# Kernel optimization log

Measured on AMD Instinct MI355X. Metric: run time of the kernel, lower is better.

The kernel has to match this reference:

```python
import jax, jax.numpy as jnp
import numpy as np

NUM_TOKENS = 16384
HIDDEN = 4096
NUM_EXPERTS = 64
TOP_K = 8


def setup_inputs() -> dict:
    key = jax.random.key(0)
    k1, k2 = jax.random.split(key)
    x = jax.random.normal(k1, (NUM_TOKENS, HIDDEN), dtype=jnp.float32)
    # nn.Linear default init scale ~ 1/sqrt(fan_in); keep logits well-scaled
    gate_w = jax.random.normal(k2, (NUM_EXPERTS, HIDDEN), dtype=jnp.float32) / jnp.sqrt(jnp.float32(HIDDEN))
    gate_b = jnp.zeros((NUM_EXPERTS,), dtype=jnp.float32)
    return {"x": x, "gate_w": gate_w, "gate_b": gate_b}


def reference(x, gate_w, gate_b):
    # gate linear: (T, H) @ (H, E) + (E,) -> (T, E)
    g = jnp.einsum("th,eh->te", x, gate_w) + gate_b
    # top-k over experts (sorted descending, like torch.topk)
    top_vals, top_idx = jax.lax.top_k(g, TOP_K)  # (T, K) each
    # softmax over the k selected logits
    expert_weights = jax.nn.softmax(top_vals, axis=-1)
    return expert_weights, top_idx
```

## Files before the change

### kernel.cpp

```cpp
#include <hip/hip_runtime.h>
#include <math.h>


#define NUM_TOKENS 16384
#define HID 4096
#define NE 64
#define TOPK 8
#define BT 32
#define BK 64
#define WSTRIDE 66

__global__ __launch_bounds__(256, 2)
void gating_kernel(const float* __restrict__ x,
                   const float* __restrict__ gw,
                   const float* __restrict__ gb,
                   float* __restrict__ out) {
    __shared__ double ws_d[NE][WSTRIDE];
    __shared__ double xs_d[BT][WSTRIDE];

    const int tid  = threadIdx.x;
    const int tok0 = blockIdx.x * BT;

    const int e0 = tid & 15;
    const int t2 = (tid >> 4) * 2;

    double acc[2][4];
#pragma unroll
    for (int i = 0; i < 2; i++)
#pragma unroll
        for (int j = 0; j < 4; j++) acc[i][j] = 0.0;

    for (int k0 = 0; k0 < HID; k0 += BK) {
#pragma unroll
        for (int i = 0; i < 2; i++) {
            int idx = i * 256 + tid;
            int tt  = idx >> 4;
            int cc  = (idx & 15) << 2;
            float4 v = *(const float4*)(x + (size_t)(tok0 + tt) * HID + k0 + cc);
            xs_d[tt][cc + 0] = (double)v.x;
            xs_d[tt][cc + 1] = (double)v.y;
            xs_d[tt][cc + 2] = (double)v.z;
            xs_d[tt][cc + 3] = (double)v.w;
        }
#pragma unroll
        for (int i = 0; i < 4; i++) {
            int idx = i * 256 + tid;
            int ee  = idx >> 4;
            int cc  = (idx & 15) << 2;
            float4 v = *(const float4*)(gw + (size_t)ee * HID + k0 + cc);
            ws_d[ee][cc + 0] = (double)v.x;
            ws_d[ee][cc + 1] = (double)v.y;
            ws_d[ee][cc + 2] = (double)v.z;
            ws_d[ee][cc + 3] = (double)v.w;
        }
        __syncthreads();

        const double* xr0 = &xs_d[t2 + 0][0];
        const double* xr1 = &xs_d[t2 + 1][0];
        const double* w0  = &ws_d[e0 +  0][0];
        const double* w1  = &ws_d[e0 + 16][0];
        const double* w2  = &ws_d[e0 + 32][0];
        const double* w3  = &ws_d[e0 + 48][0];

#pragma unroll 8
        for (int kk = 0; kk < BK; kk++) {
            double xa = xr0[kk], xb = xr1[kk];
            double a0 = w0[kk], a1 = w1[kk], a2 = w2[kk], a3 = w3[kk];
            acc[0][0] = fma(xa, a0, acc[0][0]);
            acc[0][1] = fma(xa, a1, acc[0][1]);
            acc[0][2] = fma(xa, a2, acc[0][2]);
            acc[0][3] = fma(xa, a3, acc[0][3]);
            acc[1][0] = fma(xb, a0, acc[1][0]);
            acc[1][1] = fma(xb, a1, acc[1][1]);
            acc[1][2] = fma(xb, a2, acc[1][2]);
            acc[1][3] = fma(xb, a3, acc[1][3]);
        }
        __syncthreads();
    }

    double* lg = &ws_d[0][0];
#pragma unroll
    for (int i = 0; i < 2; i++) {
        int t = t2 + i;
#pragma unroll
        for (int j = 0; j < 4; j++) {
            int e = e0 + 16 * j;
            lg[t * 65 + e] = acc[i][j] + (double)gb[e];
        }
    }
    __syncthreads();

    const int wv = tid >> 6, ln = tid & 63;
    if (ln < 8) {
        int t = wv * 8 + ln;
        const double* row = lg + t * 65;
        unsigned long long sel = 0ull;
        double vals[TOPK];
        int idxs[TOPK];
#pragma unroll
        for (int k = 0; k < TOPK; k++) {
            double bv = -1e300;
            int bi = 0;
            for (int e = 0; e < NE; e++) {
                bool valid = !((sel >> e) & 1ull);
                double v = row[e];
                bool take = valid && (v > bv);
                bv = take ? v : bv;
                bi = take ? e : bi;
            }
            sel |= 1ull << bi;
            vals[k] = bv;
            idxs[k] = bi;
        }
        double m = vals[0];
        float ex[TOPK];
        float s = 0.f;
#pragma unroll
        for (int k = 0; k < TOPK; k++) {
            ex[k] = expf((float)(vals[k] - m));
            s += ex[k];
        }
        float inv = 1.0f / s;
        float* ow = out;
        float* oi = out + NUM_TOKENS * TOPK;
        int gt = tok0 + t;
#pragma unroll
        for (int k = 0; k < TOPK; k++) {
            ow[gt * TOPK + k] = ex[k] * inv;
            oi[gt * TOPK + k] = (float)idxs[k];
        }
    }
}

extern "C" void kernel_launch(void* const* d_in, const int* in_sizes, int n_in,
                              void* d_out, int out_size, void* d_ws, size_t ws_size,
                              hipStream_t stream) {
    const float* x  = (const float*)d_in[0];
    const float* gw = (const float*)d_in[1];
    const float* gb = (const float*)d_in[2];
    float* out = (float*)d_out;

    dim3 grid(NUM_TOKENS / BT);
    dim3 block(256);
    gating_kernel<<<grid, block, 0, stream>>>(x, gw, gb, out);
}
```

Before: 597.5 us.

## Compute gating logits in fp32 with fp64 chunk accumulation and margin-based fp64 recompute

Replaces the all-fp64 tiled GEMM with fp32 FMAs over 16-element sub-chunks that are accumulated into fp64 per expert. Each thread now handles one token and 8 experts, reading weights directly from global memory (cached) and prefetching x chunks into registers. It adds a fallback: tokens whose top-9 logit gaps fall below a margin have their logits recomputed exactly in fp64 across the whole block before the final top-k. This swaps the slow fp64 arithmetic for fp32 throughput, at the cost of extra branching and serialized recomputes for near-tie tokens.

```diff
diff --git a/kernel.cpp b/kernel.cpp
--- a/kernel.cpp
+++ b/kernel.cpp
@@ -2,128 +2,170 @@
 #include <math.h>
 
 
-#define NUM_TOKENS 16384
+#define NT 16384
 #define HID 4096
 #define NE 64
 #define TOPK 8
-#define BT 32
-#define BK 64
-#define WSTRIDE 66
+#define BT 64
+#define CK 64
+#define NCH (HID / CK)
+#define XS_S 68
+#define LG_S 65
+#define MARGIN 1e-3
 
-__global__ __launch_bounds__(256, 2)
+__device__ __forceinline__ void scan_top(const double* row, double* vals, int* idxs, int np) {
+    unsigned long long sel = 0ull;
+    for (int kk = 0; kk < np; kk++) {
+        double bv = -1e300;
+        int bi = 0;
+        for (int e = 0; e < NE; e++) {
+            bool valid = !((sel >> e) & 1ull);
+            double v = row[e];
+            bool take = valid && (v > bv);
+            bv = take ? v : bv;
+            bi = take ? e : bi;
+        }
+        sel |= 1ull << bi;
+        vals[kk] = bv;
+        idxs[kk] = bi;
+    }
+}
+
+__global__ __launch_bounds__(512, 2)
 void gating_kernel(const float* __restrict__ x,
                    const float* __restrict__ gw,
                    const float* __restrict__ gb,
                    float* __restrict__ out) {
-    __shared__ double ws_d[NE][WSTRIDE];
-    __shared__ double xs_d[BT][WSTRIDE];
+    __shared__ union {
+        float  xs[BT * XS_S];
+        double lg[BT * LG_S];
+    } u;
+    __shared__ double pp[NE * 9];
+    __shared__ int flags[BT];
 
     const int tid  = threadIdx.x;
+    const int ln   = tid & 63;
+    const int wv   = __builtin_amdgcn_readfirstlane(tid >> 6);
+    const int eb   = wv * 8;
     const int tok0 = blockIdx.x * BT;
 
-    const int e0 = tid & 15;
-    const int t2 = (tid >> 4) * 2;
+    float4 px[2];
+#pragma unroll
+    for (int i = 0; i < 2; i++) {
+        int idx = i * 512 + tid, r = idx >> 4, c = (idx & 15) << 2;
+        px[i] = *(const float4*)(x + (size_t)(tok0 + r) * HID + c);
+    }
 
-    double acc[2][4];
+    double dacc[8];
 #pragma unroll
-    for (int i = 0; i < 2; i++)
-#pragma unroll
-        for (int j = 0; j < 4; j++) acc[i][j] = 0.0;
+    for (int e = 0; e < 8; e++) dacc[e] = 0.0;
 
-    for (int k0 = 0; k0 < HID; k0 += BK) {
+    for (int ch = 0; ch < NCH; ch++) {
+        __syncthreads();
 #pragma unroll
         for (int i = 0; i < 2; i++) {
-            int idx = i * 256 + tid;
-            int tt  = idx >> 4;
-            int cc  = (idx & 15) << 2;
-            float4 v = *(const float4*)(x + (size_t)(tok0 + tt) * HID + k0 + cc);
-            xs_d[tt][cc + 0] = (double)v.x;
-            xs_d[tt][cc + 1] = (double)v.y;
-            xs_d[tt][cc + 2] = (double)v.z;
-            xs_d[tt][cc + 3] = (double)v.w;
-        }
-#pragma unroll
-        for (int i = 0; i < 4; i++) {
-            int idx = i * 256 + tid;
-            int ee  = idx >> 4;
-            int cc  = (idx & 15) << 2;
-            float4 v = *(const float4*)(gw + (size_t)ee * HID + k0 + cc);
-            ws_d[ee][cc + 0] = (double)v.x;
-            ws_d[ee][cc + 1] = (double)v.y;
-            ws_d[ee][cc + 2] = (double)v.z;
-            ws_d[ee][cc + 3] = (double)v.w;
+            int idx = i * 512 + tid, r = idx >> 4, c = (idx & 15) << 2;
+            *(float4*)(&u.xs[r * XS_S + c]) = px[i];
         }
         __syncthreads();
+        if (ch + 1 < NCH) {
+            const int k0n = (ch + 1) * CK;
+#pragma unroll
+            for (int i = 0; i < 2; i++) {
+                int idx = i * 512 + tid, r = idx >> 4, c = (idx & 15) << 2;
+                px[i] = *(const float4*)(x + (size_t)(tok0 + r) * HID + k0n + c);
+            }
+        }
 
-        const double* xr0 = &xs_d[t2 + 0][0];
-        const double* xr1 = &xs_d[t2 + 1][0];
-        const double* w0  = &ws_d[e0 +  0][0];
-        const double* w1  = &ws_d[e0 + 16][0];
-        const double* w2  = &ws_d[e0 + 32][0];
-        const double* w3  = &ws_d[e0 + 48][0];
-
-#pragma unroll 8
-        for (int kk = 0; kk < BK; kk++) {
-            double xa = xr0[kk], xb = xr1[kk];
-            double a0 = w0[kk], a1 = w1[kk], a2 = w2[kk], a3 = w3[kk];
-            acc[0][0] = fma(xa, a0, acc[0][0]);
-            acc[0][1] = fma(xa, a1, acc[0][1]);
-            acc[0][2] = fma(xa, a2, acc[0][2]);
-            acc[0][3] = fma(xa, a3, acc[0][3]);
-            acc[1][0] = fma(xb, a0, acc[1][0]);
-            acc[1][1] = fma(xb, a1, acc[1][1]);
-            acc[1][2] = fma(xb, a2, acc[1][2]);
-            acc[1][3] = fma(xb, a3, acc[1][3]);
+        const float* xrow  = &u.xs[ln * XS_S];
+        const float* wbase = gw + (size_t)eb * HID + ch * CK;
+#pragma unroll
+        for (int q = 0; q < 4; q++) {
+            float f[8];
+#pragma unroll
+            for (int e = 0; e < 8; e++) f[e] = 0.f;
+#pragma unroll
+            for (int g = 0; g < 4; g++) {
+                const int k = q * 16 + g * 4;
+                float4 xv = *(const float4*)(xrow + k);
+#pragma unroll
+                for (int e = 0; e < 8; e++) {
+                    float4 w4 = *(const float4*)(wbase + (size_t)e * HID + k);
+                    f[e] = fmaf(xv.x, w4.x, f[e]);
+                    f[e] = fmaf(xv.y, w4.y, f[e]);
+                    f[e] = fmaf(xv.z, w4.z, f[e]);
+                    f[e] = fmaf(xv.w, w4.w, f[e]);
+                }
+            }
+#pragma unroll
+            for (int e = 0; e < 8; e++) dacc[e] += (double)f[e];
         }
-        __syncthreads();
     }
 
-    double* lg = &ws_d[0][0];
+    __syncthreads();
+    {
+        double* lgrow = &u.lg[ln * LG_S + eb];
 #pragma unroll
-    for (int i = 0; i < 2; i++) {
-        int t = t2 + i;
-#pragma unroll
-        for (int j = 0; j < 4; j++) {
-            int e = e0 + 16 * j;
-            lg[t * 65 + e] = acc[i][j] + (double)gb[e];
-        }
+        for (int e = 0; e < 8; e++) lgrow[e] = dacc[e] + (double)gb[eb + e];
     }
     __syncthreads();
 
-    const int wv = tid >> 6, ln = tid & 63;
-    if (ln < 8) {
-        int t = wv * 8 + ln;
-        const double* row = lg + t * 65;
-        unsigned long long sel = 0ull;
-        double vals[TOPK];
-        int idxs[TOPK];
+    double vals[9];
+    int idxs[9];
+    int myflag = 0;
+    if (wv == 0) {
+        scan_top(&u.lg[ln * LG_S], vals, idxs, 9);
+        double mg = 1e300;
+#pragma unroll
+        for (int kk = 0; kk < 8; kk++) {
+            double g = vals[kk] - vals[kk + 1];
+            mg = (g < mg) ? g : mg;
+        }
+        myflag = (mg < MARGIN) ? 1 : 0;
+        flags[ln] = myflag;
+    }
+    __syncthreads();
+
+    for (int t = 0; t < BT; t++) {
+        if (flags[t]) {
+            const int e  = tid & 63;
+            const int sl = wv;
+            const float* xr = x  + (size_t)(tok0 + t) * HID + sl * 512;
+            const float* wr = gw + (size_t)e * HID + sl * 512;
+            double p0 = 0., p1 = 0., p2 = 0., p3 = 0.;
+            for (int kk = 0; kk < 512; kk += 4) {
+                float4 a = *(const float4*)(xr + kk);
+                float4 b = *(const float4*)(wr + kk);
+                p0 = fma((double)a.x, (double)b.x, p0);
+                p1 = fma((double)a.y, (double)b.y, p1);
+                p2 = fma((double)a.z, (double)b.z, p2);
+                p3 = fma((double)a.w, (double)b.w, p3);
+            }
+            pp[e * 9 + sl] = (p0 + p1) + (p2 + p3);
+            __syncthreads();
+            if (tid < 64) {
+                double s = (double)gb[tid];
+#pragma unroll
+                for (int s2 = 0; s2 < 8; s2++) s += pp[tid * 9 + s2];
+                u.lg[t * LG_S + tid] = s;
+            }
+            __syncthreads();
+        }
+    }
+
+    if (wv == 0) {
+        if (myflag) scan_top(&u.lg[ln * LG_S], vals, idxs, 8);
+        double mx = vals[0];
+        float ex[TOPK], s = 0.f;
 #pragma unroll
         for (int k = 0; k < TOPK; k++) {
-            double bv = -1e300;
-            int bi = 0;
-            for (int e = 0; e < NE; e++) {
-                bool valid = !((sel >> e) & 1ull);
-                double v = row[e];
-                bool take = valid && (v > bv);
-                bv = take ? v : bv;
-                bi = take ? e : bi;
-            }
-            sel |= 1ull << bi;
-            vals[k] = bv;
-            idxs[k] = bi;
-        }
-        double m = vals[0];
-        float ex[TOPK];
-        float s = 0.f;
-#pragma unroll
-        for (int k = 0; k < TOPK; k++) {
-            ex[k] = expf((float)(vals[k] - m));
+            ex[k] = expf((float)(vals[k] - mx));
             s += ex[k];
         }
         float inv = 1.0f / s;
         float* ow = out;
-        float* oi = out + NUM_TOKENS * TOPK;
-        int gt = tok0 + t;
+        float* oi = out + NT * TOPK;
+        int gt = tok0 + ln;
 #pragma unroll
         for (int k = 0; k < TOPK; k++) {
             ow[gt * TOPK + k] = ex[k] * inv;
@@ -140,7 +182,7 @@
     const float* gb = (const float*)d_in[2];
     float* out = (float*)d_out;
 
-    dim3 grid(NUM_TOKENS / BT);
-    dim3 block(256);
+    dim3 grid(NT / BT);
+    dim3 block(512);
     gating_kernel<<<grid, block, 0, stream>>>(x, gw, gb, out);
 }
```

After: 981.0 us. 1.64x slower.
